# Kernel optimization log

Hardware: AMD Instinct MI355X
Metric: run time of the kernel (lower is better)

The kernel has to match this reference:

```python
import jax, jax.numpy as jnp
import numpy as np

B, N, L, M, F = 32, 32, 512, 64, 64
EPS = 1e-8

def setup_inputs() -> dict:
    key = jax.random.key(0)
    k1, k2, k3, k4, k5 = jax.random.split(key, 5)
    x_aug = jax.random.normal(k1, (B, N, L, F), dtype=jnp.float32)
    # monotone time grid in [0,1], shape (L,1) so it broadcasts against (1,N,1,M)
    t = jnp.linspace(0.0, 1.0, L, dtype=jnp.float32)[:, None]
    t_left = jax.random.uniform(k2, (N, M), dtype=jnp.float32) * 0.8
    t_right = t_left + 0.05 + 0.15 * jax.random.uniform(k3, (N, M), dtype=jnp.float32)
    kappa = jax.random.normal(k4, (N, 1), dtype=jnp.float32)
    return {"x_aug": x_aug, "t": t, "t_left": t_left, "t_right": t_right, "kappa": kappa}

def reference(x_aug, t, t_left, t_right, kappa):
    # kappa: (N,1) -> softplus -> (1,N,1,1)
    k = jax.nn.softplus(kappa)[None, :, None]          # (1,N,1,1)
    tl = t_left[None, :, None, :]                       # (1,N,1,M)
    tr = t_right[None, :, None, :]                      # (1,N,1,M)
    # soft box kernel over time: alpha (1,N,L,M)
    alpha = jax.nn.sigmoid((tr - t) / k) * jax.nn.sigmoid((t - tl) / k)
    # weighted pool over L without materializing (B,N,L,M,F)
    numerator = jnp.einsum('bnlf,nlm->bnmf', x_aug, alpha[0])  # (B,N,M,F)
    denominator = alpha.sum(axis=2)[..., None]                 # (1,N,M,1)
    return numerator / (denominator + EPS)
```

## Files before the change

kernel.cpp:

```cpp
#include <hip/hip_runtime.h>
#include <math.h>

typedef unsigned short u16;
typedef unsigned int   u32;
typedef __attribute__((ext_vector_type(8))) short short8;
typedef __attribute__((ext_vector_type(4))) float f32x4;

namespace {
constexpr int Bb = 32, Nn = 32, Ll = 512, Mm = 64, Ff = 64;
constexpr int TL  = 32;
constexpr int NT  = Ll / TL;
constexpr int TLP = 40;
constexpr float EPSV = 1e-8f;
}

__device__ __forceinline__ u16 bf16rne(float x) {
    u32 u = __float_as_uint(x);
    return (u16)((u + 0x7fffu + ((u >> 16) & 1u)) >> 16);
}
__device__ __forceinline__ float bf16tof(u16 h) {
    return __uint_as_float(((u32)h) << 16);
}

__device__ __forceinline__ void lgkm_barrier() {
    asm volatile("s_waitcnt lgkmcnt(0)" ::: "memory");
    __builtin_amdgcn_s_barrier();
    asm volatile("" ::: "memory");
}

__global__ __launch_bounds__(256, 4)
void wagg_fused2(const float* __restrict__ x_aug,
                 const float* __restrict__ t_in,
                 const float* __restrict__ t_left,
                 const float* __restrict__ t_right,
                 const float* __restrict__ kappa,
                 float* __restrict__ out)
{
    const int n   = blockIdx.x & 31;
    const int b   = blockIdx.x >> 5;
    const int tid = threadIdx.x;

    __shared__ u16 ah_s[2][Mm * TLP];
    __shared__ u16 al_s[2][Mm * TLP];
    __shared__ u16 xh_s[2][Ff * TLP];
    __shared__ u16 xl_s[2][Ff * TLP];

    const int fq  = tid & 15;
    const int lp2 = tid >> 4;
    const int sw    = (fq >> 1) & 3;
    const u32 wbase = (u32)(((lp2 >> 2) ^ sw) * 8 + (lp2 & 3) * 2);

    const int wv   = tid >> 6;
    const int lane = tid & 63;
    const int ma   = wv * 16 + (lane >> 2);
    const int lqa  = lane & 3;

    const int mh = wv & 1;
    const int fh = wv >> 1;
    const int q  = lane >> 4;
    const int c  = lane & 15;

    const float* xb = x_aug + (size_t)(b * Nn + n) * (Ll * Ff);

    const float kap = kappa[n];
    const float kk  = fmaxf(kap, 0.0f) + log1pf(expf(-fabsf(kap)));
    const float ik  = 1.0f / kk;
    const float tlv = t_left [n * Mm + ma];
    const float trv = t_right[n * Mm + ma];
    const float Ac  = __expf(-trv * ik);
    const float Bc  = __expf( tlv * ik);

    f32x4 acc[2][2];
    #pragma unroll
    for (int mi = 0; mi < 2; ++mi)
        #pragma unroll
        for (int fi = 0; fi < 2; ++fi)
            acc[mi][fi] = (f32x4){0.f, 0.f, 0.f, 0.f};

    float XA0[4], XA1[4], XB0[4], XB1[4];
    float T[8];
    float dsum = 0.0f;

#define LOADX(X0_, X1_, T_) { \
    const float* p_ = xb + (size_t)((T_) * TL + 2 * lp2) * Ff + fq * 4; \
    *(float4*)(X0_) = *(const float4*)p_; \
    *(float4*)(X1_) = *(const float4*)(p_ + Ff); }

#define LOADT(T_) { \
    *(float4*)&T[0] = *(const float4*)&t_in[(T_) * TL + lqa * 8]; \
    *(float4*)&T[4] = *(const float4*)&t_in[(T_) * TL + lqa * 8 + 4]; }

#define STAGEX(BUF_, X0_, X1_) { \
    _Pragma("unroll") \
    for (int j = 0; j < 4; ++j) { \
        const float v0 = (X0_)[j], v1 = (X1_)[j]; \
        const u16 h0 = bf16rne(v0), h1 = bf16rne(v1); \
        const u16 s0 = bf16rne(v0 - bf16tof(h0)), s1 = bf16rne(v1 - bf16tof(h1)); \
        const u32 off_ = (u32)(fq * 4 + j) * TLP + wbase; \
        *(u32*)&xh_s[BUF_][off_] = (u32)h0 | ((u32)h1 << 16); \
        *(u32*)&xl_s[BUF_][off_] = (u32)s0 | ((u32)s1 << 16); } \
    u32 hi_[4], lo_[4]; \
    _Pragma("unroll") \
    for (int jj = 0; jj < 8; jj += 2) { \
        const float u0 = __expf(T[jj]     * ik); \
        const float u1 = __expf(T[jj + 1] * ik); \
        const float d0 = fmaf(Ac, u0, 1.0f) * (u0 + Bc); \
        const float d1 = fmaf(Ac, u1, 1.0f) * (u1 + Bc); \
        const float a0 = u0 * __builtin_amdgcn_rcpf(d0); \
        const float a1 = u1 * __builtin_amdgcn_rcpf(d1); \
        dsum += a0 + a1; \
        const u16 h0 = bf16rne(a0), h1 = bf16rne(a1); \
        const u16 s0 = bf16rne(a0 - bf16tof(h0)), s1 = bf16rne(a1 - bf16tof(h1)); \
        hi_[jj >> 1] = (u32)h0 | ((u32)h1 << 16); \
        lo_[jj >> 1] = (u32)s0 | ((u32)s1 << 16); } \
    const u32 aoff_ = (u32)ma * TLP + lqa * 8; \
    *(uint4*)&ah_s[BUF_][aoff_] = make_uint4(hi_[0], hi_[1], hi_[2], hi_[3]); \
    *(uint4*)&al_s[BUF_][aoff_] = make_uint4(lo_[0], lo_[1], lo_[2], lo_[3]); }

#define TILE(T_, CUR_, XS0_, XS1_, XL0_, XL1_) { \
    if ((T_) + 1 < NT) LOADT((T_) + 1); \
    if ((T_) + 2 < NT) LOADX(XL0_, XL1_, (T_) + 2); \
    short8 ahf[2], alf[2], xhf[2], xlf[2]; \
    _Pragma("unroll") \
    for (int mi = 0; mi < 2; ++mi) { \
        const u32 off_ = (u32)(mh * 32 + mi * 16 + c) * TLP + q * 8; \
        ahf[mi] = *(const short8*)&ah_s[CUR_][off_]; \
        alf[mi] = *(const short8*)&al_s[CUR_][off_]; } \
    _Pragma("unroll") \
    for (int fi = 0; fi < 2; ++fi) { \
        const int row_ = fh * 32 + fi * 16 + c; \
        const u32 off_ = (u32)row_ * TLP + (u32)((q ^ ((row_ >> 3) & 3)) * 8); \
        xhf[fi] = *(const short8*)&xh_s[CUR_][off_]; \
        xlf[fi] = *(const short8*)&xl_s[CUR_][off_]; } \
    _Pragma("unroll") \
    for (int mi = 0; mi < 2; ++mi) \
        _Pragma("unroll") \
        for (int fi = 0; fi < 2; ++fi) { \
            acc[mi][fi] = __builtin_amdgcn_mfma_f32_16x16x32_bf16(ahf[mi], xhf[fi], acc[mi][fi], 0, 0, 0); \
            acc[mi][fi] = __builtin_amdgcn_mfma_f32_16x16x32_bf16(ahf[mi], xlf[fi], acc[mi][fi], 0, 0, 0); \
            acc[mi][fi] = __builtin_amdgcn_mfma_f32_16x16x32_bf16(alf[mi], xhf[fi], acc[mi][fi], 0, 0, 0); } \
    if ((T_) + 1 < NT) STAGEX((CUR_) ^ 1, XS0_, XS1_); \
    lgkm_barrier(); }

    LOADX(XA0, XA1, 0);
    LOADT(0);
    STAGEX(0, XA0, XA1);
    LOADX(XB0, XB1, 1);
    lgkm_barrier();

    for (int tt = 0; tt < NT / 2; ++tt) {
        const int t0 = 2 * tt;
        TILE(t0,     0, XB0, XB1, XA0, XA1);
        TILE(t0 + 1, 1, XA0, XA1, XB0, XB1);
    }

#undef TILE
#undef STAGEX
#undef LOADT
#undef LOADX

    float* dred = (float*)&xh_s[0][0];
    float* invp = dred + 256;
    dred[lqa * 64 + ma] = dsum;
    lgkm_barrier();
    if (tid < Mm) {
        const float d = dred[tid] + dred[64 + tid] + dred[128 + tid] + dred[192 + tid];
        invp[tid] = __builtin_amdgcn_rcpf(d + EPSV);
    }
    lgkm_barrier();

    float* ob = out + (size_t)(b * Nn + n) * (Mm * Ff);
    #pragma unroll
    for (int mi = 0; mi < 2; ++mi) {
        const int mbase = mh * 32 + mi * 16 + q * 4;
        float iv[4];
        #pragma unroll
        for (int r = 0; r < 4; ++r) iv[r] = invp[mbase + r];
        #pragma unroll
        for (int fi = 0; fi < 2; ++fi) {
            const int f = fh * 32 + fi * 16 + c;
            #pragma unroll
            for (int r = 0; r < 4; ++r)
                ob[(size_t)(mbase + r) * Ff + f] = acc[mi][fi][r] * iv[r];
        }
    }
}

extern "C" void kernel_launch(void* const* d_in, const int* in_sizes, int n_in,
                              void* d_out, int out_size, void* d_ws, size_t ws_size,
                              hipStream_t stream)
{
    const float* x_aug   = (const float*)d_in[0];
    const float* t_in    = (const float*)d_in[1];
    const float* t_left  = (const float*)d_in[2];
    const float* t_right = (const float*)d_in[3];
    const float* kappa   = (const float*)d_in[4];
    float* out = (float*)d_out;

    hipLaunchKernelGGL(wagg_fused2, dim3(Bb * Nn), dim3(256), 0, stream,
                       x_aug, t_in, t_left, t_right, kappa, out);
}
```

Measured before the change: 207.2 us.

## Split feature dimension across two blocks and single-buffer LDS

Each (b,n) problem is now handled by two blocks, each covering half of the F dimension. That doubles the grid to 2048 blocks, and the launch bound rises to 6 blocks per CU. The LDS double buffering is replaced by a single buffer, with an extra barrier between fragment reads and the restage. The x prefetch depth drops from two tiles to one. Both blocks recompute the alpha weights, so that work is duplicated. Each block also loads half-row 128-byte segments, and the x staging now uses scalar 16-bit LDS stores.

```diff
diff --git a/kernel.cpp b/kernel.cpp
--- a/kernel.cpp
+++ b/kernel.cpp
@@ -11,6 +11,7 @@
 constexpr int TL  = 32;
 constexpr int NT  = Ll / TL;
 constexpr int TLP = 40;
+constexpr int FH  = 32;
 constexpr float EPSV = 1e-8f;
 }
 
@@ -28,27 +29,28 @@
     asm volatile("" ::: "memory");
 }
 
-__global__ __launch_bounds__(256, 4)
-void wagg_fused2(const float* __restrict__ x_aug,
+__global__ __launch_bounds__(256, 6)
+void wagg_fsplit(const float* __restrict__ x_aug,
                  const float* __restrict__ t_in,
                  const float* __restrict__ t_left,
                  const float* __restrict__ t_right,
                  const float* __restrict__ kappa,
                  float* __restrict__ out)
 {
-    const int n   = blockIdx.x & 31;
-    const int b   = blockIdx.x >> 5;
-    const int tid = threadIdx.x;
+    const int fhalf = blockIdx.x & 1;
+    const int n     = (blockIdx.x >> 1) & 31;
+    const int b     = blockIdx.x >> 6;
+    const int tid   = threadIdx.x;
 
-    __shared__ u16 ah_s[2][Mm * TLP];
-    __shared__ u16 al_s[2][Mm * TLP];
-    __shared__ u16 xh_s[2][Ff * TLP];
-    __shared__ u16 xl_s[2][Ff * TLP];
+    __shared__ u16 ah_s[Mm * TLP];
+    __shared__ u16 al_s[Mm * TLP];
+    __shared__ u16 xh_s[FH * TLP];
+    __shared__ u16 xl_s[FH * TLP];
 
-    const int fq  = tid & 15;
-    const int lp2 = tid >> 4;
-    const int sw    = (fq >> 1) & 3;
-    const u32 wbase = (u32)(((lp2 >> 2) ^ sw) * 8 + (lp2 & 3) * 2);
+    const int xfq    = tid & 7;
+    const int xl     = tid >> 3;
+    const int xchunk = xl >> 3;
+    const int xrem   = xl & 7;
 
     const int wv   = tid >> 6;
     const int lane = tid & 63;
@@ -60,7 +62,7 @@
     const int q  = lane >> 4;
     const int c  = lane & 15;
 
-    const float* xb = x_aug + (size_t)(b * Nn + n) * (Ll * Ff);
+    const float* xb = x_aug + (size_t)(b * Nn + n) * (Ll * Ff) + fhalf * FH;
 
     const float kap = kappa[n];
     const float kk  = fmaxf(kap, 0.0f) + log1pf(expf(-fabsf(kap)));
@@ -70,35 +72,33 @@
     const float Ac  = __expf(-trv * ik);
     const float Bc  = __expf( tlv * ik);
 
-    f32x4 acc[2][2];
-    #pragma unroll
-    for (int mi = 0; mi < 2; ++mi)
-        #pragma unroll
-        for (int fi = 0; fi < 2; ++fi)
-            acc[mi][fi] = (f32x4){0.f, 0.f, 0.f, 0.f};
+    f32x4 acc[2];
+    acc[0] = (f32x4){0.f, 0.f, 0.f, 0.f};
+    acc[1] = (f32x4){0.f, 0.f, 0.f, 0.f};
 
-    float XA0[4], XA1[4], XB0[4], XB1[4];
+    float X[4];
     float T[8];
     float dsum = 0.0f;
 
-#define LOADX(X0_, X1_, T_) { \
-    const float* p_ = xb + (size_t)((T_) * TL + 2 * lp2) * Ff + fq * 4; \
-    *(float4*)(X0_) = *(const float4*)p_; \
-    *(float4*)(X1_) = *(const float4*)(p_ + Ff); }
+#define LOADX(T_) { \
+    const float* p_ = xb + (size_t)((T_) * TL + xl) * Ff + xfq * 4; \
+    *(float4*)X = *(const float4*)p_; }
 
 #define LOADT(T_) { \
     *(float4*)&T[0] = *(const float4*)&t_in[(T_) * TL + lqa * 8]; \
     *(float4*)&T[4] = *(const float4*)&t_in[(T_) * TL + lqa * 8 + 4]; }
 
-#define STAGEX(BUF_, X0_, X1_) { \
+#define STAGE() { \
     _Pragma("unroll") \
     for (int j = 0; j < 4; ++j) { \
-        const float v0 = (X0_)[j], v1 = (X1_)[j]; \
-        const u16 h0 = bf16rne(v0), h1 = bf16rne(v1); \
-        const u16 s0 = bf16rne(v0 - bf16tof(h0)), s1 = bf16rne(v1 - bf16tof(h1)); \
-        const u32 off_ = (u32)(fq * 4 + j) * TLP + wbase; \
-        *(u32*)&xh_s[BUF_][off_] = (u32)h0 | ((u32)h1 << 16); \
-        *(u32*)&xl_s[BUF_][off_] = (u32)s0 | ((u32)s1 << 16); } \
+        const float v = X[j]; \
+        const u16 h = bf16rne(v); \
+        const u16 s = bf16rne(v - bf16tof(h)); \
+        const int row_ = xfq * 4 + j; \
+        const u32 off_ = (u32)row_ * TLP \
+                       + (u32)(((xchunk ^ ((row_ >> 3) & 3)) * 8) + xrem); \
+        xh_s[off_] = h; \
+        xl_s[off_] = s; } \
     u32 hi_[4], lo_[4]; \
     _Pragma("unroll") \
     for (int jj = 0; jj < 8; jj += 2) { \
@@ -114,52 +114,44 @@
         hi_[jj >> 1] = (u32)h0 | ((u32)h1 << 16); \
         lo_[jj >> 1] = (u32)s0 | ((u32)s1 << 16); } \
     const u32 aoff_ = (u32)ma * TLP + lqa * 8; \
-    *(uint4*)&ah_s[BUF_][aoff_] = make_uint4(hi_[0], hi_[1], hi_[2], hi_[3]); \
-    *(uint4*)&al_s[BUF_][aoff_] = make_uint4(lo_[0], lo_[1], lo_[2], lo_[3]); }
+    *(uint4*)&ah_s[aoff_] = make_uint4(hi_[0], hi_[1], hi_[2], hi_[3]); \
+    *(uint4*)&al_s[aoff_] = make_uint4(lo_[0], lo_[1], lo_[2], lo_[3]); }
 
-#define TILE(T_, CUR_, XS0_, XS1_, XL0_, XL1_) { \
-    if ((T_) + 1 < NT) LOADT((T_) + 1); \
-    if ((T_) + 2 < NT) LOADX(XL0_, XL1_, (T_) + 2); \
-    short8 ahf[2], alf[2], xhf[2], xlf[2]; \
-    _Pragma("unroll") \
-    for (int mi = 0; mi < 2; ++mi) { \
-        const u32 off_ = (u32)(mh * 32 + mi * 16 + c) * TLP + q * 8; \
-        ahf[mi] = *(const short8*)&ah_s[CUR_][off_]; \
-        alf[mi] = *(const short8*)&al_s[CUR_][off_]; } \
-    _Pragma("unroll") \
-    for (int fi = 0; fi < 2; ++fi) { \
-        const int row_ = fh * 32 + fi * 16 + c; \
-        const u32 off_ = (u32)row_ * TLP + (u32)((q ^ ((row_ >> 3) & 3)) * 8); \
-        xhf[fi] = *(const short8*)&xh_s[CUR_][off_]; \
-        xlf[fi] = *(const short8*)&xl_s[CUR_][off_]; } \
-    _Pragma("unroll") \
-    for (int mi = 0; mi < 2; ++mi) \
-        _Pragma("unroll") \
-        for (int fi = 0; fi < 2; ++fi) { \
-            acc[mi][fi] = __builtin_amdgcn_mfma_f32_16x16x32_bf16(ahf[mi], xhf[fi], acc[mi][fi], 0, 0, 0); \
-            acc[mi][fi] = __builtin_amdgcn_mfma_f32_16x16x32_bf16(ahf[mi], xlf[fi], acc[mi][fi], 0, 0, 0); \
-            acc[mi][fi] = __builtin_amdgcn_mfma_f32_16x16x32_bf16(alf[mi], xhf[fi], acc[mi][fi], 0, 0, 0); } \
-    if ((T_) + 1 < NT) STAGEX((CUR_) ^ 1, XS0_, XS1_); \
-    lgkm_barrier(); }
-
-    LOADX(XA0, XA1, 0);
+    LOADX(0);
     LOADT(0);
-    STAGEX(0, XA0, XA1);
-    LOADX(XB0, XB1, 1);
+    STAGE();
     lgkm_barrier();
 
-    for (int tt = 0; tt < NT / 2; ++tt) {
-        const int t0 = 2 * tt;
-        TILE(t0,     0, XB0, XB1, XA0, XA1);
-        TILE(t0 + 1, 1, XA0, XA1, XB0, XB1);
+    for (int t = 0; t < NT; ++t) {
+        if (t + 1 < NT) { LOADX(t + 1); LOADT(t + 1); }
+
+        short8 ahf[2], alf[2], xhf, xlf;
+        #pragma unroll
+        for (int mi = 0; mi < 2; ++mi) {
+            const u32 off = (u32)(mh * 32 + mi * 16 + c) * TLP + q * 8;
+            ahf[mi] = *(const short8*)&ah_s[off];
+            alf[mi] = *(const short8*)&al_s[off];
+        }
+        {
+            const int row = fh * 16 + c;
+            const u32 off = (u32)row * TLP + (u32)((q ^ ((row >> 3) & 3)) * 8);
+            xhf = *(const short8*)&xh_s[off];
+            xlf = *(const short8*)&xl_s[off];
+        }
+        lgkm_barrier();
+
+        #pragma unroll
+        for (int mi = 0; mi < 2; ++mi) {
+            acc[mi] = __builtin_amdgcn_mfma_f32_16x16x32_bf16(ahf[mi], xhf, acc[mi], 0, 0, 0);
+            acc[mi] = __builtin_amdgcn_mfma_f32_16x16x32_bf16(ahf[mi], xlf, acc[mi], 0, 0, 0);
+            acc[mi] = __builtin_amdgcn_mfma_f32_16x16x32_bf16(alf[mi], xhf, acc[mi], 0, 0, 0);
+        }
+
+        if (t + 1 < NT) STAGE();
+        lgkm_barrier();
     }
 
-#undef TILE
-#undef STAGEX
-#undef LOADT
-#undef LOADX
-
-    float* dred = (float*)&xh_s[0][0];
+    float* dred = (float*)&xh_s[0];
     float* invp = dred + 256;
     dred[lqa * 64 + ma] = dsum;
     lgkm_barrier();
@@ -169,21 +161,22 @@
     }
     lgkm_barrier();
 
-    float* ob = out + (size_t)(b * Nn + n) * (Mm * Ff);
+    float* ob = out + (size_t)(b * Nn + n) * (Mm * Ff) + fhalf * FH;
     #pragma unroll
     for (int mi = 0; mi < 2; ++mi) {
         const int mbase = mh * 32 + mi * 16 + q * 4;
         float iv[4];
         #pragma unroll
         for (int r = 0; r < 4; ++r) iv[r] = invp[mbase + r];
+        const int f = fh * 16 + c;
         #pragma unroll
-        for (int fi = 0; fi < 2; ++fi) {
-            const int f = fh * 32 + fi * 16 + c;
-            #pragma unroll
-            for (int r = 0; r < 4; ++r)
-                ob[(size_t)(mbase + r) * Ff + f] = acc[mi][fi][r] * iv[r];
-        }
+        for (int r = 0; r < 4; ++r)
+            ob[(size_t)(mbase + r) * Ff + f] = acc[mi][r] * iv[r];
     }
+
+#undef STAGE
+#undef LOADT
+#undef LOADX
 }
 
 extern "C" void kernel_launch(void* const* d_in, const int* in_sizes, int n_in,
@@ -197,6 +190,6 @@
     const float* kappa   = (const float*)d_in[4];
     float* out = (float*)d_out;
 
-    hipLaunchKernelGGL(wagg_fused2, dim3(Bb * Nn), dim3(256), 0, stream,
+    hipLaunchKernelGGL(wagg_fsplit, dim3(Bb * Nn * 2), dim3(256), 0, stream,
                        x_aug, t_in, t_left, t_right, kappa, out);
 }
```

Result: no change. 204.6 us (-1.3%).
